# Kernel tuning notes

Measured on AMD Instinct MI355X. Metric: run time of the kernel, lower is better.

Reference implementation:

```python
import jax, jax.numpy as jnp
import numpy as np
import math

B, T, C = 2, 1400, 256
H = 16
D = C // H            # 16
FF = 1024
VOCAB = 1400
SLOTS = 256
EPS = 1e-5


def _ln(x, g, b):
    m = jnp.mean(x, axis=-1, keepdims=True)
    v = jnp.mean(jnp.square(x - m), axis=-1, keepdims=True)
    return (x - m) * jax.lax.rsqrt(v + EPS) * g + b


def setup_inputs() -> dict:
    key = jax.random.key(0)
    ks = jax.random.split(key, 24)
    s = 0.02
    inp = {
        "x": jax.random.normal(ks[0], (B, T, C), dtype=jnp.float32),
        "disease_ids": jax.random.randint(ks[1], (B, T), 0, VOCAB),
        # nn.MultiheadAttention params (torch layout: [out,in])
        "in_proj_w": jax.random.normal(ks[2], (3 * C, C)) * s,
        "in_proj_b": jnp.zeros((3 * C,), jnp.float32),
        "out_proj_w": jax.random.normal(ks[3], (C, C)) * s,
        "out_proj_b": jnp.zeros((C,), jnp.float32),
        # LayerNorms
        "ln1_g": jnp.ones((C,), jnp.float32), "ln1_b": jnp.zeros((C,), jnp.float32),
        "ln2_g": jnp.ones((C,), jnp.float32), "ln2_b": jnp.zeros((C,), jnp.float32),
        "ln3_g": jnp.ones((C,), jnp.float32), "ln3_b": jnp.zeros((C,), jnp.float32),
        # DiseaseGraphAttention
        "gq_w": jax.random.normal(ks[4], (C, C)) * s, "gq_b": jnp.zeros((C,), jnp.float32),
        "gk_w": jax.random.normal(ks[5], (C, C)) * s, "gk_b": jnp.zeros((C,), jnp.float32),
        "gv_w": jax.random.normal(ks[6], (C, C)) * s, "gv_b": jnp.zeros((C,), jnp.float32),
        "go_w": jax.random.normal(ks[7], (C, C)) * s, "go_b": jnp.zeros((C,), jnp.float32),
        "affinity": jax.random.normal(ks[8], (VOCAB, VOCAB)) * 0.01,
        # LongTermMemoryBank (only the read path affects the returned output)
        "mem_bank": jax.random.normal(ks[9], (SLOTS, C)) * 0.1,
        "read_w": jax.random.normal(ks[10], (SLOTS, C)) * s,
        "read_b": jnp.zeros((SLOTS,), jnp.float32),
        # FFN
        "ffn_w1": jax.random.normal(ks[11], (FF, C)) * s, "ffn_b1": jnp.zeros((FF,), jnp.float32),
        "ffn_w2": jax.random.normal(ks[12], (C, FF)) * s, "ffn_b2": jnp.zeros((C,), jnp.float32),
    }
    return inp


def reference(x, disease_ids, in_proj_w, in_proj_b, out_proj_w, out_proj_b,
              ln1_g, ln1_b, ln2_g, ln2_b, ln3_g, ln3_b,
              gq_w, gq_b, gk_w, gk_b, gv_w, gv_b, go_w, go_b, affinity,
              mem_bank, read_w, read_b, ffn_w1, ffn_b1, ffn_w2, ffn_b2):
    scale = 1.0 / math.sqrt(D)

    # ---- standard MHA (pre-norm, residual), dropout in eval mode ----
    h = _ln(x, ln1_g, ln1_b)
    qkv = h @ in_proj_w.T + in_proj_b                      # [B,T,3C]
    q, k, v = jnp.split(qkv, 3, axis=-1)
    q = q.reshape(B, T, H, D); k = k.reshape(B, T, H, D); v = v.reshape(B, T, H, D)
    scores = jnp.einsum('bthd,bshd->bhts', q, k) * scale   # [B,H,T,T]
    attn = jax.nn.softmax(scores, axis=-1)
    o = jnp.einsum('bhts,bshd->bthd', attn, v).reshape(B, T, C)
    x = x + (o @ out_proj_w.T + out_proj_b)

    # ---- disease-graph attention with gathered affinity bias ----
    h = _ln(x, ln2_g, ln2_b)
    q = (h @ gq_w.T + gq_b).reshape(B, T, H, D)
    k = (h @ gk_w.T + gk_b).reshape(B, T, H, D)
    v = (h @ gv_w.T + gv_b).reshape(B, T, H, D)
    aff = affinity[disease_ids]                            # [B,T,VOCAB] (VOCAB == T)
    scores = jnp.einsum('bthd,bshd->bhts', q, k) * scale + aff[:, None, :, :] * 0.1
    attn = jax.nn.softmax(scores, axis=-1)
    o = jnp.einsum('bhts,bshd->bthd', attn, v).reshape(B, T, C)
    x = x + (o @ go_w.T + go_b)

    # ---- memory-bank read (write/erase only mutate params, not the output) ----
    read_weights = jax.nn.softmax(x @ read_w.T + read_b, axis=-1)   # [B,T,SLOTS]
    x = x + jnp.einsum('bts,sc->btc', read_weights, mem_bank)

    # ---- FFN ----
    h = _ln(x, ln3_g, ln3_b)
    ff = jax.nn.gelu(h @ ffn_w1.T + ffn_b1, approximate=False) @ ffn_w2.T + ffn_b2
    return x + ff
```

## Files before the change

### kernel.cpp

```cpp
#include <hip/hip_runtime.h>
#include <hip/hip_bf16.h>
#include <math.h>

namespace {

typedef __attribute__((ext_vector_type(4))) float f32x4;
typedef __attribute__((ext_vector_type(8))) short s16x8;
typedef __attribute__((ext_vector_type(4))) short s16x4;
typedef unsigned short ushort_t;

constexpr int kB = 2, kT = 1400, kC = 256, kH = 16, kFF = 1024;
constexpr int kBT = kB * kT;
constexpr float kEps = 1e-5f;
constexpr int kSP = 5;
constexpr int kSLen = 280;
constexpr int SBLK = 288;
constexpr int KPITCH = 24;

__device__ __forceinline__ ushort_t f2bf(float f) {
    unsigned u = __float_as_uint(f);
    u += 0x7fffu + ((u >> 16) & 1u);
    return (ushort_t)(u >> 16);
}
__device__ __forceinline__ float bf2f(ushort_t u) {
    return __uint_as_float(((unsigned)u) << 16);
}
__device__ __forceinline__ unsigned pk2bf(float a, float b) {
    __hip_bfloat162 t = __float22bfloat162_rn(make_float2(a, b));
    union { __hip_bfloat162 h; unsigned u; } cv; cv.h = t;
    return cv.u;
}

__global__ __launch_bounds__(256) void convert_kernel(
        const float* __restrict__ in_proj_w, const float* __restrict__ gq_w,
        const float* __restrict__ gk_w, const float* __restrict__ gv_w,
        const float* __restrict__ out_proj_w, const float* __restrict__ go_w,
        const float* __restrict__ ffn_w1, const float* __restrict__ ffn_w2,
        const float* __restrict__ read_w, const float* __restrict__ mem_bank,
        const float* __restrict__ gq_b, const float* __restrict__ gk_b,
        const float* __restrict__ gv_b,
        ushort_t* __restrict__ wdst, float* __restrict__ gqkvb) {
    const int bid = blockIdx.x, tid = threadIdx.x;
    if (bid == 608) {
        gqkvb[tid] = gq_b[tid];
        gqkvb[256 + tid] = gk_b[tid];
        gqkvb[512 + tid] = gv_b[tid];
        return;
    }
    const int u0 = (bid * 256 + tid) * 8;
    if (u0 >= 1114112) {
        #pragma unroll
        for (int j = 0; j < 8; j++) {
            const int d = u0 - 1114112 + j;
            wdst[1114112 + d] = f2bf(mem_bank[(d & 255) * 256 + (d >> 8)]);
        }
        return;
    }
    const float* src; int off;
    if      (u0 < 196608)  { src = in_proj_w;  off = u0; }
    else if (u0 < 262144)  { src = gq_w;       off = u0 - 196608; }
    else if (u0 < 327680)  { src = gk_w;       off = u0 - 262144; }
    else if (u0 < 393216)  { src = gv_w;       off = u0 - 327680; }
    else if (u0 < 458752)  { src = out_proj_w; off = u0 - 393216; }
    else if (u0 < 524288)  { src = go_w;       off = u0 - 458752; }
    else if (u0 < 786432)  { src = ffn_w1;     off = u0 - 524288; }
    else if (u0 < 1048576) { src = ffn_w2;     off = u0 - 786432; }
    else                   { src = read_w;     off = u0 - 1048576; }
    #pragma unroll
    for (int j = 0; j < 8; j++) wdst[u0 + j] = f2bf(src[off + j]);
}

__global__ __launch_bounds__(256) void ln_kernel(
        const float* __restrict__ x, const float* __restrict__ g,
        const float* __restrict__ b, ushort_t* __restrict__ out) {
    __shared__ float red[10];
    const int row = blockIdx.x, tid = threadIdx.x;
    const float v = x[row * kC + tid];
    float s1 = v, s2 = v * v;
    #pragma unroll
    for (int off = 32; off > 0; off >>= 1) {
        s1 += __shfl_down(s1, off);
        s2 += __shfl_down(s2, off);
    }
    if ((tid & 63) == 0) { red[tid >> 6] = s1; red[4 + (tid >> 6)] = s2; }
    __syncthreads();
    if (tid == 0) {
        red[8] = red[0] + red[1] + red[2] + red[3];
        red[9] = red[4] + red[5] + red[6] + red[7];
    }
    __syncthreads();
    const float mean = red[8] * (1.f / kC);
    const float var = red[9] * (1.f / kC) - mean * mean;
    out[row * kC + tid] = f2bf((v - mean) * rsqrtf(var + kEps) * g[tid] + b[tid]);
}

__global__ __launch_bounds__(256) void softmax256_kernel(
        const float* __restrict__ logits, ushort_t* __restrict__ probs) {
    __shared__ float red[5];
    const int row = blockIdx.x, tid = threadIdx.x;
    const float p = __expf(logits[row * 256 + tid]);
    float s = p;
    #pragma unroll
    for (int off = 32; off > 0; off >>= 1) s += __shfl_down(s, off);
    if ((tid & 63) == 0) red[tid >> 6] = s;
    __syncthreads();
    if (tid == 0) red[4] = red[0] + red[1] + red[2] + red[3];
    __syncthreads();
    probs[row * 256 + tid] = f2bf(p / red[4]);
}

__global__ __launch_bounds__(256) void gemm16_kernel(
        const ushort_t* __restrict__ A, const ushort_t* __restrict__ W,
        const float* __restrict__ bias, const float* __restrict__ res,
        float* __restrict__ outf, ushort_t* __restrict__ outb,
        ushort_t* __restrict__ outK, ushort_t* __restrict__ outV,
        int M, int N, int K, int ldo, int act, int mode) {
    __shared__ ushort_t dsA[64 * 64];
    __shared__ ushort_t dsW[64 * 64];
    const int tid = threadIdx.x;
    const int lane = tid & 63, wave = tid >> 6;
    const int qi = lane & 15, g = lane >> 4;
    const int wm = (wave >> 1) * 32, wn = (wave & 1) * 32;
    const int m0 = blockIdx.x * 64, n0 = blockIdx.y * 64;

    f32x4 acc[2][2] = {};
    for (int kt = 0; kt < K; kt += 64) {
        __syncthreads();
        #pragma unroll
        for (int j = 0; j < 2; ++j) {
            const int u = tid + j * 256;
            const int row = u >> 3, c = u & 7;
            const int cs = c ^ (row & 7);
            const int gmA = min(m0 + row, M - 1);
            *(s16x8*)&dsA[row * 64 + cs * 8] =
                *(const s16x8*)&A[(size_t)gmA * K + kt + c * 8];
            *(s16x8*)&dsW[row * 64 + cs * 8] =
                *(const s16x8*)&W[(size_t)(n0 + row) * K + kt + c * 8];
        }
        __syncthreads();
        #pragma unroll
        for (int kk = 0; kk < 2; ++kk) {
            s16x8 af[2], bf[2];
            #pragma unroll
            for (int f = 0; f < 2; ++f) {
                const int r = wm + f * 16 + qi;
                af[f] = *(const s16x8*)&dsA[r * 64 + (((kk * 4 + g) ^ (r & 7)) * 8)];
            }
            #pragma unroll
            for (int nn = 0; nn < 2; ++nn) {
                const int r = wn + nn * 16 + qi;
                bf[nn] = *(const s16x8*)&dsW[r * 64 + (((kk * 4 + g) ^ (r & 7)) * 8)];
            }
            #pragma unroll
            for (int f = 0; f < 2; ++f)
                #pragma unroll
                for (int nn = 0; nn < 2; ++nn)
                    acc[f][nn] = __builtin_amdgcn_mfma_f32_16x16x32_bf16(
                        af[f], bf[nn], acc[f][nn], 0, 0, 0);
        }
    }
    #pragma unroll
    for (int f = 0; f < 2; ++f) {
        #pragma unroll
        for (int r = 0; r < 4; ++r) {
            const int gm = m0 + wm + f * 16 + g * 4 + r;
            if (gm >= M) continue;
            #pragma unroll
            for (int nn = 0; nn < 2; ++nn) {
                const int gn = n0 + wn + nn * 16 + qi;
                float v = acc[f][nn][r];
                if (bias) v += bias[gn];
                if (act == 1) v = 0.5f * v * (1.f + erff(v * 0.70710678f));
                if (res) v += res[(size_t)gm * ldo + gn];
                if (mode == 1) {
                    const int bb = (gm >= kT) ? 1 : 0;
                    const int ss = gm - bb * kT;
                    const int hh = (gn & 255) >> 4, dd = gn & 15;
                    const size_t hoff = (((size_t)(bb * 16 + hh)) * kT + ss) * 16 + dd;
                    if (gn < 256)      outb[hoff] = f2bf(v * 0.25f);
                    else if (gn < 512) outK[hoff] = f2bf(v);
                    else               outV[hoff] = f2bf(v);
                } else {
                    if (outf) outf[(size_t)gm * ldo + gn] = v;
                    if (outb) outb[(size_t)gm * ldo + gn] = f2bf(v);
                }
            }
        }
    }
}

template <bool kAff>
__global__ __launch_bounds__(512) void attn_mfma_kernel(
        const ushort_t* __restrict__ q, const ushort_t* __restrict__ kbuf,
        const ushort_t* __restrict__ vbuf, ushort_t* __restrict__ o_part,
        float* __restrict__ l_part,
        const float* __restrict__ affinity, const int* __restrict__ did) {
    __shared__ ushort_t ldsK[SBLK * KPITCH];
    __shared__ ushort_t ldsV[SBLK * 16];
    const int tid  = threadIdx.x;
    const int bid  = blockIdx.x;
    const int w    = (bid & 7) * 220 + (bid >> 3);
    const int slice = w / 11;
    const int ttile = w - slice * 11;
    const int h    = slice & 15;
    const int z    = slice >> 4;
    const int b    = (z >= 5) ? 1 : 0;
    const int sp   = z - b * 5;
    const int t0   = ttile * 128;
    const int s0   = sp * kSLen;
    const int lane = tid & 63;
    const int wave = tid >> 6;
    const int g    = lane >> 4;
    const int qi   = lane & 15;

    const int tq  = t0 + wave * 16 + qi;
    const int tqc = min(tq, kT - 1);
    const ushort_t* qhb = q + (size_t)(b * 16 + h) * kT * 16;
    s16x8 qb = {0, 0, 0, 0, 0, 0, 0, 0};
    if (g < 2) qb = *(const s16x8*)&qhb[(size_t)tqc * 16 + g * 8];
    const float* ar = nullptr;
    if (kAff) ar = affinity + (size_t)did[b * kT + tqc] * kT;

    const ushort_t* kb  = kbuf + (size_t)(b * 16 + h) * kT * 16;
    const ushort_t* vbp = vbuf + (size_t)(b * 16 + h) * kT * 16;
    for (int i = tid; i < SBLK * 2; i += 512) {
        const int sl = i >> 1, hf = i & 1;
        const int sg = min(s0 + sl, kT - 1);
        *(s16x8*)&ldsK[sl * KPITCH + hf * 8] =
            *(const s16x8*)&kb[(size_t)sg * 16 + hf * 8];
        *(s16x8*)&ldsV[sl * 16 + hf * 8] =
            *(const s16x8*)&vbp[(size_t)sg * 16 + hf * 8];
    }
    __syncthreads();

    f32x4 acc = {0.f, 0.f, 0.f, 0.f};
    float lrun = 0.f;
    const unsigned vaddr = (unsigned)(size_t)(&ldsV[0]) + lane * 8;

    for (int c = 0; c < SBLK / 32; ++c) {
        const int sl0 = c * 32;
        const bool tail = (c == 8);
        s16x8 ka0 = {0, 0, 0, 0, 0, 0, 0, 0};
        s16x8 ka1 = {0, 0, 0, 0, 0, 0, 0, 0};
        if (g < 2) {
            ka0 = *(const s16x8*)&ldsK[(sl0 + qi) * KPITCH + g * 8];
            ka1 = *(const s16x8*)&ldsK[(sl0 + 16 + qi) * KPITCH + g * 8];
        }
        const f32x4 z4 = {0.f, 0.f, 0.f, 0.f};
        f32x4 d0 = __builtin_amdgcn_mfma_f32_16x16x32_bf16(ka0, qb, z4, 0, 0, 0);
        f32x4 d1 = __builtin_amdgcn_mfma_f32_16x16x32_bf16(ka1, qb, z4, 0, 0, 0);
        float sv[8];
        #pragma unroll
        for (int r = 0; r < 4; r++) { sv[r] = d0[r]; sv[4 + r] = d1[r]; }
        if (kAff) {
            if (!tail) {
                const float4 a0 = *(const float4*)&ar[s0 + sl0 + 4 * g];
                const float4 a1 = *(const float4*)&ar[s0 + sl0 + 16 + 4 * g];
                sv[0] += 0.1f * a0.x; sv[1] += 0.1f * a0.y;
                sv[2] += 0.1f * a0.z; sv[3] += 0.1f * a0.w;
                sv[4] += 0.1f * a1.x; sv[5] += 0.1f * a1.y;
                sv[6] += 0.1f * a1.z; sv[7] += 0.1f * a1.w;
            } else {
                #pragma unroll
                for (int jj = 0; jj < 8; jj++) {
                    const int s_ = s0 + sl0 + 16 * (jj >> 2) + 4 * g + (jj & 3);
                    sv[jj] += 0.1f * ar[min(s_, kT - 1)];
                }
            }
        }
        float pv[8];
        #pragma unroll
        for (int jj = 0; jj < 8; jj++) pv[jj] = __expf(sv[jj]);
        if (tail && g >= 2) { pv[4] = 0.f; pv[5] = 0.f; pv[6] = 0.f; pv[7] = 0.f; }
        lrun += ((pv[0] + pv[1]) + (pv[2] + pv[3])) + ((pv[4] + pv[5]) + (pv[6] + pv[7]));
        union { unsigned u[4]; s16x8 s; } pu;
        pu.u[0] = pk2bf(pv[0], pv[1]);
        pu.u[1] = pk2bf(pv[2], pv[3]);
        pu.u[2] = pk2bf(pv[4], pv[5]);
        pu.u[3] = pk2bf(pv[6], pv[7]);
        s16x4 va0, va1;
        asm volatile("ds_read_b64_tr_b16 %0, %2\n\t"
                     "ds_read_b64_tr_b16 %1, %2 offset:512\n\t"
                     "s_waitcnt lgkmcnt(0)"
                     : "=&v"(va0), "=&v"(va1)
                     : "v"(vaddr + sl0 * 32));
        __builtin_amdgcn_sched_barrier(0);
        s16x8 af;
        #pragma unroll
        for (int j = 0; j < 4; j++) { af[j] = va0[j]; af[4 + j] = va1[j]; }
        acc = __builtin_amdgcn_mfma_f32_16x16x32_bf16(af, pu.s, acc, 0, 0, 0);
    }
    lrun += __shfl_xor(lrun, 16);
    lrun += __shfl_xor(lrun, 32);
    const int slice_id = (b * kSP + sp) * 16 + h;
    if (lane < 16 && tq < kT)
        l_part[(size_t)slice_id * kT + tq] = lrun;
    ushort_t* ob = o_part + (size_t)slice_id * kT * 16;
    s16x4 ov;
    #pragma unroll
    for (int r = 0; r < 4; r++) ov[r] = (short)f2bf(acc[r]);
    if (tq < kT) *(s16x4*)&ob[(size_t)tq * 16 + 4 * g] = ov;
}

__global__ __launch_bounds__(256) void combine_kernel(
        const ushort_t* __restrict__ o_part, const float* __restrict__ l_part,
        ushort_t* __restrict__ o) {
    const int row = blockIdx.x, c = threadIdx.x;
    const int b = (row >= kT) ? 1 : 0, t = row - b * kT;
    const int h = c >> 4, d = c & 15;
    float l = 0.f, ov = 0.f;
    #pragma unroll
    for (int p = 0; p < kSP; ++p) {
        const int sl_ = (b * kSP + p) * 16 + h;
        l  += l_part[(size_t)sl_ * kT + t];
        ov += bf2f(o_part[((size_t)sl_ * kT + t) * 16 + d]);
    }
    o[(size_t)row * 256 + c] = f2bf(ov / l);
}

}

extern "C" void kernel_launch(void* const* d_in, const int* in_sizes, int n_in,
                              void* d_out, int out_size, void* d_ws, size_t ws_size,
                              hipStream_t stream) {
    const float* x          = (const float*)d_in[0];
    const int*   did        = (const int*)d_in[1];
    const float* in_proj_w  = (const float*)d_in[2];
    const float* in_proj_b  = (const float*)d_in[3];
    const float* out_proj_w = (const float*)d_in[4];
    const float* out_proj_b = (const float*)d_in[5];
    const float* ln1_g = (const float*)d_in[6];
    const float* ln1_b = (const float*)d_in[7];
    const float* ln2_g = (const float*)d_in[8];
    const float* ln2_b = (const float*)d_in[9];
    const float* ln3_g = (const float*)d_in[10];
    const float* ln3_b = (const float*)d_in[11];
    const float* gq_w = (const float*)d_in[12];
    const float* gq_b = (const float*)d_in[13];
    const float* gk_w = (const float*)d_in[14];
    const float* gk_b = (const float*)d_in[15];
    const float* gv_w = (const float*)d_in[16];
    const float* gv_b = (const float*)d_in[17];
    const float* go_w = (const float*)d_in[18];
    const float* go_b = (const float*)d_in[19];
    const float* affinity = (const float*)d_in[20];
    const float* mem_bank = (const float*)d_in[21];
    const float* read_w   = (const float*)d_in[22];
    const float* read_b   = (const float*)d_in[23];
    const float* ffn_w1 = (const float*)d_in[24];
    const float* ffn_b1 = (const float*)d_in[25];
    const float* ffn_w2 = (const float*)d_in[26];
    const float* ffn_b2 = (const float*)d_in[27];

    char* wsb = (char*)d_ws;
    ushort_t* o_part  = (ushort_t*)(wsb + 0);
    float*    l_part  = (float*)(wsb + 7168000);
    ushort_t* ff116   = (ushort_t*)(wsb + 8064000);
    float*    bufD    = (float*)(wsb + 13798400);
    ushort_t* bufA16  = (ushort_t*)(wsb + 16665600);
    float*    bufD2   = (float*)(wsb + 18099200);
    ushort_t* bufQ16  = (ushort_t*)(wsb + 20966400);
    ushort_t* bufK16  = (ushort_t*)(wsb + 22400000);
    ushort_t* bufV16  = (ushort_t*)(wsb + 23833600);
    ushort_t* o16     = (ushort_t*)(wsb + 25267200);
    ushort_t* wdst    = (ushort_t*)(wsb + 26700800);
    float*    gqkvb   = (float*)(wsb + 29191168);
    float*    logits  = (float*)(wsb + 20966400);
    ushort_t* probs16 = o16;
    ushort_t* bufD16  = bufA16;

    const ushort_t* wQKV1 = wdst;
    const ushort_t* wG    = wdst + 196608;
    const ushort_t* wO    = wdst + 393216;
    const ushort_t* wGO   = wdst + 458752;
    const ushort_t* wF1   = wdst + 524288;
    const ushort_t* wF2   = wdst + 786432;
    const ushort_t* wRead = wdst + 1048576;
    const ushort_t* wMemT = wdst + 1114112;

    const dim3 blk(256);
    const int MT = (kBT + 63) / 64;
    const dim3 g_qkv(MT, 12), g_c(MT, 4), g_ff(MT, 16);
    const dim3 g_at(11 * kH * kB * kSP);

    convert_kernel<<<609, blk, 0, stream>>>(in_proj_w, gq_w, gk_w, gv_w, out_proj_w,
                                            go_w, ffn_w1, ffn_w2, read_w, mem_bank,
                                            gq_b, gk_b, gv_b, wdst, gqkvb);
    ln_kernel<<<kBT, blk, 0, stream>>>(x, ln1_g, ln1_b, bufA16);
    gemm16_kernel<<<g_qkv, blk, 0, stream>>>(bufA16, wQKV1, in_proj_b, nullptr,
                                             nullptr, bufQ16, bufK16, bufV16,
                                             kBT, 768, kC, 768, 0, 1);
    attn_mfma_kernel<false><<<g_at, dim3(512), 0, stream>>>(bufQ16, bufK16, bufV16,
                                                            o_part, l_part,
                                                            nullptr, nullptr);
    combine_kernel<<<kBT, blk, 0, stream>>>(o_part, l_part, o16);
    gemm16_kernel<<<g_c, blk, 0, stream>>>(o16, wO, out_proj_b, x,
                                           bufD2, nullptr, nullptr, nullptr,
                                           kBT, kC, kC, kC, 0, 0);
    ln_kernel<<<kBT, blk, 0, stream>>>(bufD2, ln2_g, ln2_b, bufA16);
    gemm16_kernel<<<g_qkv, blk, 0, stream>>>(bufA16, wG, gqkvb, nullptr,
                                             nullptr, bufQ16, bufK16, bufV16,
                                             kBT, 768, kC, 768, 0, 1);
    attn_mfma_kernel<true><<<g_at, dim3(512), 0, stream>>>(bufQ16, bufK16, bufV16,
                                                           o_part, l_part,
                                                           affinity, did);
    combine_kernel<<<kBT, blk, 0, stream>>>(o_part, l_part, o16);
    gemm16_kernel<<<g_c, blk, 0, stream>>>(o16, wGO, go_b, bufD2,
                                           bufD, bufD16, nullptr, nullptr,
                                           kBT, kC, kC, kC, 0, 0);
    gemm16_kernel<<<g_c, blk, 0, stream>>>(bufD16, wRead, read_b, nullptr,
                                           logits, nullptr, nullptr, nullptr,
                                           kBT, kC, kC, kC, 0, 0);
    softmax256_kernel<<<kBT, blk, 0, stream>>>(logits, probs16);
    gemm16_kernel<<<g_c, blk, 0, stream>>>(probs16, wMemT, nullptr, bufD,
                                           bufD, nullptr, nullptr, nullptr,
                                           kBT, kC, kC, kC, 0, 0);
    ln_kernel<<<kBT, blk, 0, stream>>>(bufD, ln3_g, ln3_b, bufA16);
    gemm16_kernel<<<g_ff, blk, 0, stream>>>(bufA16, wF1, ffn_b1, nullptr,
                                            nullptr, ff116, nullptr, nullptr,
                                            kBT, kFF, kC, kFF, 1, 0);
    gemm16_kernel<<<g_c, blk, 0, stream>>>(ff116, wF2, ffn_b2, bufD,
                                           (float*)d_out, nullptr, nullptr, nullptr,
                                           kBT, kC, kFF, kC, 0, 0);
}
```

Baseline: 179.1 us.

## Prefetch V transposed reads, use exp2 with folded log2e, unroll attention loop

Moves the transposed LDS reads of V one iteration ahead so they overlap with the score MFMA and softmax math, and fully unrolls the chunk loop. Folds log2(e) into the Q scale and the affinity scale so the exponential becomes a raw v_exp_f32. Also drops the g<2 branch on K loads, relying on the zero-padded Q operand to cancel the extra lanes. The risks are added register pressure from the unroll, and correctness of the inline-asm waitcnt ordering if the compiler places the prefetched read after the asm wait.

```diff
diff --git a/kernel.cpp b/kernel.cpp
--- a/kernel.cpp
+++ b/kernel.cpp
@@ -16,6 +16,8 @@
 constexpr int kSLen = 280;
 constexpr int SBLK = 288;
 constexpr int KPITCH = 24;
+constexpr float kQScale   = 0.25f * 1.4426950408889634f;
+constexpr float kAffScale = 0.1f * 1.4426950408889634f;
 
 __device__ __forceinline__ ushort_t f2bf(float f) {
     unsigned u = __float_as_uint(f);
@@ -29,6 +31,11 @@
     __hip_bfloat162 t = __float22bfloat162_rn(make_float2(a, b));
     union { __hip_bfloat162 h; unsigned u; } cv; cv.h = t;
     return cv.u;
+}
+__device__ __forceinline__ float fast_exp2(float x) {
+    float r;
+    asm("v_exp_f32 %0, %1" : "=v"(r) : "v"(x));
+    return r;
 }
 
 __global__ __launch_bounds__(256) void convert_kernel(
@@ -177,7 +184,7 @@
                     const int ss = gm - bb * kT;
                     const int hh = (gn & 255) >> 4, dd = gn & 15;
                     const size_t hoff = (((size_t)(bb * 16 + hh)) * kT + ss) * 16 + dd;
-                    if (gn < 256)      outb[hoff] = f2bf(v * 0.25f);
+                    if (gn < 256)      outb[hoff] = f2bf(v * kQScale);
                     else if (gn < 512) outK[hoff] = f2bf(v);
                     else               outV[hoff] = f2bf(v);
                 } else {
@@ -236,16 +243,17 @@
     f32x4 acc = {0.f, 0.f, 0.f, 0.f};
     float lrun = 0.f;
     const unsigned vaddr = (unsigned)(size_t)(&ldsV[0]) + lane * 8;
-
+    s16x4 va0, va1;
+    asm volatile("ds_read_b64_tr_b16 %0, %2\n\t"
+                 "ds_read_b64_tr_b16 %1, %2 offset:512"
+                 : "=&v"(va0), "=&v"(va1) : "v"(vaddr));
+
+    #pragma unroll
     for (int c = 0; c < SBLK / 32; ++c) {
         const int sl0 = c * 32;
         const bool tail = (c == 8);
-        s16x8 ka0 = {0, 0, 0, 0, 0, 0, 0, 0};
-        s16x8 ka1 = {0, 0, 0, 0, 0, 0, 0, 0};
-        if (g < 2) {
-            ka0 = *(const s16x8*)&ldsK[(sl0 + qi) * KPITCH + g * 8];
-            ka1 = *(const s16x8*)&ldsK[(sl0 + 16 + qi) * KPITCH + g * 8];
-        }
+        const s16x8 ka0 = *(const s16x8*)&ldsK[(sl0 + qi) * KPITCH + (g & 1) * 8];
+        const s16x8 ka1 = *(const s16x8*)&ldsK[(sl0 + 16 + qi) * KPITCH + (g & 1) * 8];
         const f32x4 z4 = {0.f, 0.f, 0.f, 0.f};
         f32x4 d0 = __builtin_amdgcn_mfma_f32_16x16x32_bf16(ka0, qb, z4, 0, 0, 0);
         f32x4 d1 = __builtin_amdgcn_mfma_f32_16x16x32_bf16(ka1, qb, z4, 0, 0, 0);
@@ -256,21 +264,21 @@
             if (!tail) {
                 const float4 a0 = *(const float4*)&ar[s0 + sl0 + 4 * g];
                 const float4 a1 = *(const float4*)&ar[s0 + sl0 + 16 + 4 * g];
-                sv[0] += 0.1f * a0.x; sv[1] += 0.1f * a0.y;
-                sv[2] += 0.1f * a0.z; sv[3] += 0.1f * a0.w;
-                sv[4] += 0.1f * a1.x; sv[5] += 0.1f * a1.y;
-                sv[6] += 0.1f * a1.z; sv[7] += 0.1f * a1.w;
+                sv[0] += kAffScale * a0.x; sv[1] += kAffScale * a0.y;
+                sv[2] += kAffScale * a0.z; sv[3] += kAffScale * a0.w;
+                sv[4] += kAffScale * a1.x; sv[5] += kAffScale * a1.y;
+                sv[6] += kAffScale * a1.z; sv[7] += kAffScale * a1.w;
             } else {
                 #pragma unroll
                 for (int jj = 0; jj < 8; jj++) {
                     const int s_ = s0 + sl0 + 16 * (jj >> 2) + 4 * g + (jj & 3);
-                    sv[jj] += 0.1f * ar[min(s_, kT - 1)];
+                    sv[jj] += kAffScale * ar[min(s_, kT - 1)];
                 }
             }
         }
         float pv[8];
         #pragma unroll
-        for (int jj = 0; jj < 8; jj++) pv[jj] = __expf(sv[jj]);
+        for (int jj = 0; jj < 8; jj++) pv[jj] = fast_exp2(sv[jj]);
         if (tail && g >= 2) { pv[4] = 0.f; pv[5] = 0.f; pv[6] = 0.f; pv[7] = 0.f; }
         lrun += ((pv[0] + pv[1]) + (pv[2] + pv[3])) + ((pv[4] + pv[5]) + (pv[6] + pv[7]));
         union { unsigned u[4]; s16x8 s; } pu;
@@ -278,17 +286,17 @@
         pu.u[1] = pk2bf(pv[2], pv[3]);
         pu.u[2] = pk2bf(pv[4], pv[5]);
         pu.u[3] = pk2bf(pv[6], pv[7]);
-        s16x4 va0, va1;
-        asm volatile("ds_read_b64_tr_b16 %0, %2\n\t"
-                     "ds_read_b64_tr_b16 %1, %2 offset:512\n\t"
-                     "s_waitcnt lgkmcnt(0)"
-                     : "=&v"(va0), "=&v"(va1)
-                     : "v"(vaddr + sl0 * 32));
+        asm volatile("s_waitcnt lgkmcnt(0)" ::: "memory");
         __builtin_amdgcn_sched_barrier(0);
         s16x8 af;
         #pragma unroll
         for (int j = 0; j < 4; j++) { af[j] = va0[j]; af[4 + j] = va1[j]; }
         acc = __builtin_amdgcn_mfma_f32_16x16x32_bf16(af, pu.s, acc, 0, 0, 0);
+        if (c < SBLK / 32 - 1) {
+            asm volatile("ds_read_b64_tr_b16 %0, %2\n\t"
+                         "ds_read_b64_tr_b16 %1, %2 offset:512"
+                         : "=&v"(va0), "=&v"(va1) : "v"(vaddr + (sl0 + 32) * 32));
+        }
     }
     lrun += __shfl_xor(lrun, 16);
     lrun += __shfl_xor(lrun, 32);
```

Result: faster. 174.5 us (-2.6%).
